# Kernel tuning notes

Measured on AMD Instinct MI355X. Metric: run time of the kernel, lower is better.

## Reference

```python
import jax, jax.numpy as jnp
import numpy as np

B, S, H = 4, 4096, 1024
GAMMA = 0.96875


def decay_mask(seq_len, gamma, dtype=jnp.float32):
    # D[i, j] = gamma**(i-j) for i >= j, else 0 (causal gamma-decay mask)
    i = jnp.arange(seq_len)[:, None]
    j = jnp.arange(seq_len)[None, :]
    exp = (i - j).astype(dtype)
    return jnp.where(i >= j, jnp.power(jnp.asarray(gamma, dtype), exp), jnp.zeros((), dtype))


def setup_inputs() -> dict:
    key = jax.random.key(0)
    ks = jax.random.split(key, 6)
    sc = 1.0 / np.sqrt(H)
    return {
        "x": jax.random.normal(ks[0], (B, S, H), dtype=jnp.float32),
        "Wq": jax.random.normal(ks[1], (H, H), dtype=jnp.float32) * sc,
        "bq": jax.random.normal(ks[2], (H,), dtype=jnp.float32) * 0.01,
        "Wk": jax.random.normal(ks[3], (H, H), dtype=jnp.float32) * sc,
        "bk": jax.random.normal(ks[4], (H,), dtype=jnp.float32) * 0.01,
        "Wv": jax.random.normal(ks[5], (H, H), dtype=jnp.float32) * sc,
    }


def reference(x, Wq, bq, Wk, bk, Wv):
    # Parallel representation of retention.
    seq_len = x.shape[1]
    q = jnp.einsum("bsh,oh->bso", x, Wq) + bq  # [B,S,H]
    k = jnp.einsum("bsh,oh->bso", x, Wk) + bk  # [B,S,H]
    v = jnp.einsum("bsh,oh->bso", x, Wv)       # [B,S,H]
    D = decay_mask(seq_len, GAMMA, x.dtype)     # [S,S]
    scores = jnp.einsum("bqh,bkh->bqk", q, k) * D[None]  # [B,S,S]
    return jnp.einsum("bqk,bkh->bqh", scores, v)
```

## Files before the change

### kernel.cpp

```cpp
#include <hip/hip_runtime.h>


typedef __attribute__((ext_vector_type(8))) short short8;
typedef __attribute__((ext_vector_type(4))) float floatx4;

#define MFMA(a, b, c) __builtin_amdgcn_mfma_f32_16x16x32_bf16((a), (b), (c), 0, 0, 0)

#define B_SZ   4
#define S_LEN  4096
#define H_DIM  1024
#define NROWS  (B_SZ * S_LEN)
#define HP     1088
#define WR     1152
#define LOG2G  (-0.045803690f)

__device__ __forceinline__ unsigned short f32_to_bf16_rn(float f) {
    unsigned int u = __float_as_uint(f);
    u += 0x7FFFu + ((u >> 16) & 1u);
    return (unsigned short)(u >> 16);
}

#define GLOAD_LDS16(gptr, lptr)                                                        \
    __builtin_amdgcn_global_load_lds((__attribute__((address_space(1))) void*)(gptr),  \
                                     (__attribute__((address_space(3))) void*)(lptr),  \
                                     16, 0, 0)

__global__ __launch_bounds__(256) void cvt_bf16(const float* __restrict__ src,
                                                unsigned short* __restrict__ dst, int n4) {
    int i = blockIdx.x * 256 + threadIdx.x;
    if (i >= n4) return;
    float4 v = ((const float4*)src)[i];
    ushort4 o;
    o.x = f32_to_bf16_rn(v.x);
    o.y = f32_to_bf16_rn(v.y);
    o.z = f32_to_bf16_rn(v.z);
    o.w = f32_to_bf16_rn(v.w);
    ((ushort4*)dst)[i] = o;
}

__global__ __launch_bounds__(256) void cvt_x(const float* __restrict__ src,
                                             unsigned short* __restrict__ dst) {
    int idx = blockIdx.x * 256 + threadIdx.x;
    int row = idx >> 7, c8 = (idx & 127) * 8;
    const float4* s = (const float4*)(src + (size_t)row * H_DIM + c8);
    float4 a = s[0], b = s[1];
    ushort4 o0, o1;
    o0.x = f32_to_bf16_rn(a.x); o0.y = f32_to_bf16_rn(a.y);
    o0.z = f32_to_bf16_rn(a.z); o0.w = f32_to_bf16_rn(a.w);
    o1.x = f32_to_bf16_rn(b.x); o1.y = f32_to_bf16_rn(b.y);
    o1.z = f32_to_bf16_rn(b.z); o1.w = f32_to_bf16_rn(b.w);
    ushort4* d = (ushort4*)(dst + (size_t)row * HP + c8);
    d[0] = o0; d[1] = o1;
}

__global__ __launch_bounds__(256) void fill_pad(unsigned short* __restrict__ dst) {
    int idx = blockIdx.x * 256 + threadIdx.x;
    int row = idx >> 3, c = idx & 7;
    uint4 v; v.x = (c == 0) ? 0x00003F80u : 0u; v.y = 0u; v.z = 0u; v.w = 0u;
    *(uint4*)(dst + (size_t)row * HP + 1024 + c * 8) = v;
}

__global__ __launch_bounds__(256) void tr_cvt(const float* __restrict__ Wsrc,
                                              const float* __restrict__ bias,
                                              unsigned short* __restrict__ dst) {
    const int tid = threadIdx.x;
    const int bx = blockIdx.x, by = blockIdx.y;
    if (by >= 32) {
        if (bx != 0) return;
        const int h0 = by * 32;
#pragma unroll
        for (int i = 0; i < 128; ++i) {
            int idx = i * 256 + tid;
            int r = idx >> 10, cc = idx & 1023;
            int h = h0 + r;
            float v = (h == 1024) ? bias[cc] : 0.0f;
            dst[(size_t)h * 1024 + cc] = f32_to_bf16_rn(v);
        }
        return;
    }
    __shared__ float Lt[128][33];
    const int w0 = bx * 128, h0 = by * 32;
#pragma unroll
    for (int i = 0; i < 16; ++i) {
        int idx = i * 256 + tid;
        int r = idx >> 5, cc = idx & 31;
        Lt[r][cc] = Wsrc[(size_t)(w0 + r) * 1024 + h0 + cc];
    }
    __syncthreads();
#pragma unroll
    for (int i = 0; i < 16; ++i) {
        int idx = i * 256 + tid;
        int hh = idx >> 7, ww = idx & 127;
        dst[(size_t)(h0 + hh) * 1024 + w0 + ww] = f32_to_bf16_rn(Lt[ww][hh]);
    }
}

template <int MODE, int SWZ>
__global__ __launch_bounds__(256) void gemm128(const unsigned short* __restrict__ A, int lda,
                                               const unsigned short* __restrict__ W, int ldw,
                                               void* __restrict__ outp, int ldo, int K, int p0,
                                               int nx) {
    __shared__ unsigned short As[2][128 * 32];
    __shared__ unsigned short Bs[2][128 * 32];

    const int tid  = threadIdx.x;
    const int lane = tid & 63;
    const int w4   = tid >> 6;
    const int wm   = w4 >> 1, wn = w4 & 1;
    const int l15  = lane & 15;
    const int q8   = (lane >> 4) * 8;
    const int q4   = (lane >> 4) * 4;

    int bx, by;
    if (SWZ) {
        const int bid = blockIdx.x;
        const int g = bid & 7, j = bid >> 3;
        by = g * 16 + j / nx;
        bx = j % nx;
    } else {
        bx = blockIdx.x; by = blockIdx.y;
    }

    int aRow0 = 0, wRow0 = 0, kStart = 0;
    const unsigned short* Ap = A;
    const unsigned short* Wp = W;
    const int tT = by;
    const int tl = tT & 31;
    int jt = 0;

    if (MODE == 0) {
        aRow0 = by * 128; wRow0 = bx * 128;
    } else if (MODE == 1) {
        aRow0 = bx * 128; wRow0 = by * 128;
    } else if (MODE == 2) {
        jt = tl - 4 + bx;
        if (jt < 0) return;
        aRow0 = tT * 128;
        wRow0 = (tT >> 5) * S_LEN + jt * 128;
    } else {
        kStart = (tl < 4) ? (4 - tl) * 128 : 0;
        Ap = A + (size_t)tT * 128 * 640;
        Wp = W + (size_t)((tT >> 5) * H_DIM + bx * 128) * S_LEN + (ptrdiff_t)(tl - 4) * 128;
    }

    floatx4 acc[4][4];
#pragma unroll
    for (int i = 0; i < 4; ++i)
#pragma unroll
        for (int j = 0; j < 4; ++j) acc[i][j] = (floatx4)0.0f;

    for (int k0 = kStart; k0 < K; k0 += 64) {
        __syncthreads();
#pragma unroll
        for (int p = 0; p < 2; ++p) {
            const int c = p * 256 + tid;
            const unsigned short* gA = Ap + (size_t)(aRow0 + (c >> 2)) * lda + k0 + (c & 3) * 8;
            const unsigned short* gW = Wp + (size_t)(wRow0 + (c >> 2)) * ldw + k0 + (c & 3) * 8;
            char* dA0 = (char*)&As[0][0] + (size_t)(p * 256 + w4 * 64) * 16;
            char* dA1 = (char*)&As[1][0] + (size_t)(p * 256 + w4 * 64) * 16;
            char* dB0 = (char*)&Bs[0][0] + (size_t)(p * 256 + w4 * 64) * 16;
            char* dB1 = (char*)&Bs[1][0] + (size_t)(p * 256 + w4 * 64) * 16;
            GLOAD_LDS16(gA,      dA0);
            GLOAD_LDS16(gA + 32, dA1);
            GLOAD_LDS16(gW,      dB0);
            GLOAD_LDS16(gW + 32, dB1);
        }
        __syncthreads();

#pragma unroll
        for (int h = 0; h < 2; ++h) {
            short8 af[4], bf[4];
#pragma unroll
            for (int mt = 0; mt < 4; ++mt)
                af[mt] = *(const short8*)(&As[h][0] + (wm * 64 + mt * 16 + l15) * 32 + q8);
#pragma unroll
            for (int nt = 0; nt < 4; ++nt)
                bf[nt] = *(const short8*)(&Bs[h][0] + (wn * 64 + nt * 16 + l15) * 32 + q8);
#pragma unroll
            for (int mt = 0; mt < 4; ++mt)
#pragma unroll
                for (int nt = 0; nt < 4; ++nt)
                    acc[mt][nt] = MFMA(af[mt], bf[nt], acc[mt][nt]);
        }
    }

#pragma unroll
    for (int nt = 0; nt < 4; ++nt) {
        const int ol = wn * 64 + nt * 16 + l15;
#pragma unroll
        for (int mt = 0; mt < 4; ++mt) {
#pragma unroll
            for (int r = 0; r < 4; ++r) {
                const int nl = wm * 64 + mt * 16 + q4 + r;
                const float v = acc[mt][nt][r];
                if (MODE == 0) {
                    const int o = wRow0 + ol;
                    if (o < p0)
                        ((unsigned short*)outp)[(size_t)(aRow0 + nl) * ldo + o] = f32_to_bf16_rn(v);
                } else if (MODE == 1) {
                    const int s = wRow0 + ol;
                    const int hh = aRow0 + nl;
                    ((unsigned short*)outp)[((size_t)(s >> 12) * H_DIM + hh) * S_LEN + (s & (S_LEN - 1))] =
                        f32_to_bf16_rn(v);
                } else if (MODE == 2) {
                    const int d = (tl - jt) * 128 + nl - ol;
                    const float pv = (d >= 0) ? v * exp2f((float)d * LOG2G) : 0.0f;
                    ((unsigned short*)outp)[(size_t)tT * (128 * 640) + (size_t)nl * 640 +
                                            (size_t)bx * 128 + ol] = f32_to_bf16_rn(pv);
                } else {
                    ((float*)outp)[(size_t)(tT * 128 + nl) * H_DIM + bx * 128 + ol] = v;
                }
            }
        }
    }
}

extern "C" void kernel_launch(void* const* d_in, const int* in_sizes, int n_in,
                              void* d_out, int out_size, void* d_ws, size_t ws_size,
                              hipStream_t stream) {
    (void)in_sizes; (void)n_in; (void)out_size; (void)ws_size;

    const float* x  = (const float*)d_in[0];
    const float* Wq = (const float*)d_in[1];
    const float* bq = (const float*)d_in[2];
    const float* Wk = (const float*)d_in[3];
    const float* bk = (const float*)d_in[4];
    const float* Wv = (const float*)d_in[5];
    float* out = (float*)d_out;

    unsigned short* xtb = (unsigned short*)d_ws;
    unsigned short* gb  = xtb + (size_t)NROWS * HP;
    unsigned short* vtb = gb  + (size_t)NROWS * HP;
    unsigned short* pb  = vtb + (size_t)NROWS * H_DIM;
    unsigned short* wqT = pb  + (size_t)128 * 128 * 640;
    unsigned short* wkT = wqT + (size_t)WR * H_DIM;
    unsigned short* p1  = wkT + (size_t)WR * H_DIM;
    unsigned short* wvb = p1  + (size_t)WR * HP;

    cvt_x<<<NROWS * 128 / 256, 256, 0, stream>>>(x, xtb);
    fill_pad<<<NROWS * 8 / 256, 256, 0, stream>>>(xtb);
    cvt_bf16<<<H_DIM * H_DIM / 4 / 256, 256, 0, stream>>>(Wv, wvb, H_DIM * H_DIM / 4);
    tr_cvt<<<dim3(8, 36), 256, 0, stream>>>(Wq, bq, wqT);
    tr_cvt<<<dim3(8, 36), 256, 0, stream>>>(Wk, bk, wkT);

    gemm128<0, 0><<<dim3(9, 9), 256, 0, stream>>>(wkT, 1024, wqT, 1024, p1, HP, 1024, HP, 0);

    gemm128<0, 1><<<9 * 128, 256, 0, stream>>>(xtb, HP, p1, HP, gb, HP, HP, HP, 9);

    gemm128<1, 1><<<8 * 128, 256, 0, stream>>>(wvb, 1024, xtb, HP, vtb, 0, 1024, 0, 8);

    gemm128<2, 1><<<5 * 128, 256, 0, stream>>>(gb, HP, xtb, HP, pb, 640, HP, 0, 5);

    gemm128<3, 1><<<8 * 128, 256, 0, stream>>>(pb, 640, vtb, S_LEN, out, H_DIM, 640, 0, 8);
}
```

Baseline: 347.0 us.

## Merge independent prep and GEMM launches into fewer combined kernels

Combines ten launches into five by grouping independent work into shared grids that dispatch on block index. The weight conversions and pad fill share one kernel, the x conversion runs alongside the small Wk·Wq GEMM, and the V-transpose GEMM runs alongside the decayed score GEMM. This cuts launch gaps and lets small or tail-heavy stages overlap on the GPU. In exchange, every block reserves the larger shared memory footprint, and cvt_x blocks in the combined grid now carry GEMM LDS allocation, which may reduce occupancy.

```diff
diff --git a/kernel.cpp b/kernel.cpp
--- a/kernel.cpp
+++ b/kernel.cpp
@@ -25,9 +25,8 @@
                                      (__attribute__((address_space(3))) void*)(lptr),  \
                                      16, 0, 0)
 
-__global__ __launch_bounds__(256) void cvt_bf16(const float* __restrict__ src,
-                                                unsigned short* __restrict__ dst, int n4) {
-    int i = blockIdx.x * 256 + threadIdx.x;
+__device__ __forceinline__ void cvt_bf16_body(int i, const float* __restrict__ src,
+                                              unsigned short* __restrict__ dst, int n4) {
     if (i >= n4) return;
     float4 v = ((const float4*)src)[i];
     ushort4 o;
@@ -38,9 +37,8 @@
     ((ushort4*)dst)[i] = o;
 }
 
-__global__ __launch_bounds__(256) void cvt_x(const float* __restrict__ src,
-                                             unsigned short* __restrict__ dst) {
-    int idx = blockIdx.x * 256 + threadIdx.x;
+__device__ __forceinline__ void cvt_x_body(int idx, const float* __restrict__ src,
+                                           unsigned short* __restrict__ dst) {
     int row = idx >> 7, c8 = (idx & 127) * 8;
     const float4* s = (const float4*)(src + (size_t)row * H_DIM + c8);
     float4 a = s[0], b = s[1];
@@ -53,18 +51,17 @@
     d[0] = o0; d[1] = o1;
 }
 
-__global__ __launch_bounds__(256) void fill_pad(unsigned short* __restrict__ dst) {
-    int idx = blockIdx.x * 256 + threadIdx.x;
+__device__ __forceinline__ void fill_pad_body(int idx, unsigned short* __restrict__ dst) {
     int row = idx >> 3, c = idx & 7;
     uint4 v; v.x = (c == 0) ? 0x00003F80u : 0u; v.y = 0u; v.z = 0u; v.w = 0u;
     *(uint4*)(dst + (size_t)row * HP + 1024 + c * 8) = v;
 }
 
-__global__ __launch_bounds__(256) void tr_cvt(const float* __restrict__ Wsrc,
-                                              const float* __restrict__ bias,
-                                              unsigned short* __restrict__ dst) {
-    const int tid = threadIdx.x;
-    const int bx = blockIdx.x, by = blockIdx.y;
+__device__ __forceinline__ void tr_cvt_body(float (&Lt)[128][33],
+                                            const float* __restrict__ Wsrc,
+                                            const float* __restrict__ bias,
+                                            unsigned short* __restrict__ dst,
+                                            int bx, int by, int tid) {
     if (by >= 32) {
         if (bx != 0) return;
         const int h0 = by * 32;
@@ -78,7 +75,6 @@
         }
         return;
     }
-    __shared__ float Lt[128][33];
     const int w0 = bx * 128, h0 = by * 32;
 #pragma unroll
     for (int i = 0; i < 16; ++i) {
@@ -95,14 +91,13 @@
     }
 }
 
-template <int MODE, int SWZ>
-__global__ __launch_bounds__(256) void gemm128(const unsigned short* __restrict__ A, int lda,
-                                               const unsigned short* __restrict__ W, int ldw,
-                                               void* __restrict__ outp, int ldo, int K, int p0,
-                                               int nx) {
-    __shared__ unsigned short As[2][128 * 32];
-    __shared__ unsigned short Bs[2][128 * 32];
-
+template <int MODE>
+__device__ __forceinline__ void gemm_body(unsigned short (&As)[2][128 * 32],
+                                          unsigned short (&Bs)[2][128 * 32],
+                                          int bx, int by,
+                                          const unsigned short* __restrict__ A, int lda,
+                                          const unsigned short* __restrict__ W, int ldw,
+                                          void* __restrict__ outp, int ldo, int K, int p0) {
     const int tid  = threadIdx.x;
     const int lane = tid & 63;
     const int w4   = tid >> 6;
@@ -110,16 +105,6 @@
     const int l15  = lane & 15;
     const int q8   = (lane >> 4) * 8;
     const int q4   = (lane >> 4) * 4;
-
-    int bx, by;
-    if (SWZ) {
-        const int bid = blockIdx.x;
-        const int g = bid & 7, j = bid >> 3;
-        by = g * 16 + j / nx;
-        bx = j % nx;
-    } else {
-        bx = blockIdx.x; by = blockIdx.y;
-    }
 
     int aRow0 = 0, wRow0 = 0, kStart = 0;
     const unsigned short* Ap = A;
@@ -215,6 +200,82 @@
     }
 }
 
+__global__ __launch_bounds__(256) void prep_small(const float* __restrict__ Wq,
+                                                  const float* __restrict__ bq,
+                                                  const float* __restrict__ Wk,
+                                                  const float* __restrict__ bk,
+                                                  const float* __restrict__ Wv,
+                                                  unsigned short* __restrict__ wqT,
+                                                  unsigned short* __restrict__ wkT,
+                                                  unsigned short* __restrict__ wvb,
+                                                  unsigned short* __restrict__ xtb) {
+    __shared__ float Lt[128][33];
+    const int t = blockIdx.x, tid = threadIdx.x;
+    if (t < 288) {
+        tr_cvt_body(Lt, Wq, bq, wqT, t & 7, t >> 3, tid);
+    } else if (t < 576) {
+        const int t2 = t - 288;
+        tr_cvt_body(Lt, Wk, bk, wkT, t2 & 7, t2 >> 3, tid);
+    } else if (t < 1600) {
+        cvt_bf16_body((t - 576) * 256 + tid, Wv, wvb, H_DIM * H_DIM / 4);
+    } else {
+        fill_pad_body((t - 1600) * 256 + tid, xtb);
+    }
+}
+
+__global__ __launch_bounds__(256) void cvtx_p1(const float* __restrict__ x,
+                                               unsigned short* __restrict__ xtb,
+                                               const unsigned short* __restrict__ wkT,
+                                               const unsigned short* __restrict__ wqT,
+                                               unsigned short* __restrict__ p1) {
+    __shared__ unsigned short As[2][128 * 32];
+    __shared__ unsigned short Bs[2][128 * 32];
+    const int t = blockIdx.x;
+    if (t < 81) {
+        gemm_body<0>(As, Bs, t % 9, t / 9, wkT, 1024, wqT, 1024, p1, HP, 1024, HP);
+    } else {
+        cvt_x_body((t - 81) * 256 + threadIdx.x, x, xtb);
+    }
+}
+
+__global__ __launch_bounds__(256) void gemm_g(const unsigned short* __restrict__ xtb,
+                                              const unsigned short* __restrict__ p1,
+                                              unsigned short* __restrict__ gb) {
+    __shared__ unsigned short As[2][128 * 32];
+    __shared__ unsigned short Bs[2][128 * 32];
+    const int bid = blockIdx.x;
+    const int g = bid & 7, j = bid >> 3;
+    gemm_body<0>(As, Bs, j % 9, g * 16 + j / 9, xtb, HP, p1, HP, gb, HP, HP, HP);
+}
+
+__global__ __launch_bounds__(256) void pb_vt(const unsigned short* __restrict__ gb,
+                                             const unsigned short* __restrict__ xtb,
+                                             const unsigned short* __restrict__ wvb,
+                                             unsigned short* __restrict__ pb,
+                                             unsigned short* __restrict__ vtb) {
+    __shared__ unsigned short As[2][128 * 32];
+    __shared__ unsigned short Bs[2][128 * 32];
+    const int t = blockIdx.x;
+    if (t < 640) {
+        const int g = t & 7, j = t >> 3;
+        gemm_body<2>(As, Bs, j % 5, g * 16 + j / 5, gb, HP, xtb, HP, pb, 640, HP, 0);
+    } else {
+        const int t2 = t - 640;
+        const int g = t2 & 7, j = t2 >> 3;
+        gemm_body<1>(As, Bs, j & 7, g * 16 + (j >> 3), wvb, 1024, xtb, HP, vtb, 0, 1024, 0);
+    }
+}
+
+__global__ __launch_bounds__(256) void gemm_out(const unsigned short* __restrict__ pb,
+                                                const unsigned short* __restrict__ vtb,
+                                                float* __restrict__ out) {
+    __shared__ unsigned short As[2][128 * 32];
+    __shared__ unsigned short Bs[2][128 * 32];
+    const int bid = blockIdx.x;
+    const int g = bid & 7, j = bid >> 3;
+    gemm_body<3>(As, Bs, j & 7, g * 16 + (j >> 3), pb, 640, vtb, S_LEN, out, H_DIM, 640, 0);
+}
+
 extern "C" void kernel_launch(void* const* d_in, const int* in_sizes, int n_in,
                               void* d_out, int out_size, void* d_ws, size_t ws_size,
                               hipStream_t stream) {
@@ -237,19 +298,9 @@
     unsigned short* p1  = wkT + (size_t)WR * H_DIM;
     unsigned short* wvb = p1  + (size_t)WR * HP;
 
-    cvt_x<<<NROWS * 128 / 256, 256, 0, stream>>>(x, xtb);
-    fill_pad<<<NROWS * 8 / 256, 256, 0, stream>>>(xtb);
-    cvt_bf16<<<H_DIM * H_DIM / 4 / 256, 256, 0, stream>>>(Wv, wvb, H_DIM * H_DIM / 4);
-    tr_cvt<<<dim3(8, 36), 256, 0, stream>>>(Wq, bq, wqT);
-    tr_cvt<<<dim3(8, 36), 256, 0, stream>>>(Wk, bk, wkT);
-
-    gemm128<0, 0><<<dim3(9, 9), 256, 0, stream>>>(wkT, 1024, wqT, 1024, p1, HP, 1024, HP, 0);
-
-    gemm128<0, 1><<<9 * 128, 256, 0, stream>>>(xtb, HP, p1, HP, gb, HP, HP, HP, 9);
-
-    gemm128<1, 1><<<8 * 128, 256, 0, stream>>>(wvb, 1024, xtb, HP, vtb, 0, 1024, 0, 8);
-
-    gemm128<2, 1><<<5 * 128, 256, 0, stream>>>(gb, HP, xtb, HP, pb, 640, HP, 0, 5);
-
-    gemm128<3, 1><<<8 * 128, 256, 0, stream>>>(pb, 640, vtb, S_LEN, out, H_DIM, 640, 0, 8);
-}
+    prep_small<<<2112, 256, 0, stream>>>(Wq, bq, Wk, bk, Wv, wqT, wkT, wvb, xtb);
+    cvtx_p1<<<81 + 8192, 256, 0, stream>>>(x, xtb, wkT, wqT, p1);
+    gemm_g<<<9 * 128, 256, 0, stream>>>(xtb, p1, gb);
+    pb_vt<<<640 + 1024, 256, 0, stream>>>(gb, xtb, wvb, pb, vtb);
+    gemm_out<<<8 * 128, 256, 0, stream>>>(pb, vtb, out);
+}
```

After: 304.3 us. 12.3% less time.
